# Kernel optimization log

Hardware: AMD Instinct MI355X
Metric: run time of the kernel (lower is better)

Reference implementation:

```python
import jax, jax.numpy as jnp
import numpy as np

MAX_FPS = 30.0
NUM_HEADS = 8


def _rope(x, times):
    # x: [B, H, T, D] with D even; interleaved rotary (even/odd pairs)
    B, H, T, D = x.shape
    inv_freq = 1.0 / (10000.0 ** (jnp.arange(0, D, 2, dtype=jnp.float32) / D))  # [D/2]
    pos = jnp.round(times * MAX_FPS)                       # [B, T]
    freqs = pos[:, :, None] * inv_freq[None, None, :]      # [B, T, D/2]
    cos = jnp.cos(freqs)[:, None, :, :]                    # [B, 1, T, D/2]
    sin = jnp.sin(freqs)[:, None, :, :]
    xp = x.reshape(B, H, T, D // 2, 2)
    x0, x1 = xp[..., 0], xp[..., 1]                        # even-index, odd-index elems
    r0 = x0 * cos - x1 * sin
    r1 = x0 * sin + x1 * cos
    return jnp.stack([r0, r1], axis=-1).reshape(B, H, T, D)


def setup_inputs() -> dict:
    key = jax.random.key(0)
    k1, k2, k3, k4, k5 = jax.random.split(key, 5)
    B, N, C = 4, 2048, 512
    x = jax.random.normal(k1, (B, N, C), dtype=jnp.float32)
    mask = jnp.zeros((B, N), dtype=jnp.float32)  # additive mask, 0 = attend
    # times in seconds; rounded to frame indices inside RoPE
    times = jax.random.uniform(k2, (B, N), dtype=jnp.float32) * (N / MAX_FPS)
    bound_qkv = float(np.sqrt(6.0 / (C + 3 * C)))
    Wqkv = jax.random.uniform(k3, (3 * C, C), minval=-bound_qkv, maxval=bound_qkv, dtype=jnp.float32)
    bound_p = float(np.sqrt(6.0 / (C + C)))
    Wproj = jax.random.uniform(k4, (C, C), minval=-bound_p, maxval=bound_p, dtype=jnp.float32)
    bproj = jnp.zeros((C,), dtype=jnp.float32)
    return {"x": x, "mask": mask, "times": times, "Wqkv": Wqkv,
            "Wproj": Wproj, "bproj": bproj, "num_cls_token": 0}


def reference(x, mask, times, Wqkv, Wproj, bproj, num_cls_token):
    B, N, C = x.shape
    H = NUM_HEADS
    Dh = C // H
    qkv = (x @ Wqkv.T).reshape(B, N, 3, H, Dh).transpose(2, 0, 3, 1, 4)  # [3,B,H,N,Dh]
    q, k, v = qkv[0], qkv[1], qkv[2]
    if num_cls_token > 0:
        c_q, q = q[:, :, :num_cls_token], q[:, :, num_cls_token:]
        c_k, k = k[:, :, :num_cls_token], k[:, :, num_cls_token:]
        t = times
        q = _rope(q, t)
        k = _rope(k, t)
        q = jnp.concatenate([c_q, q], axis=2)
        k = jnp.concatenate([c_k, k], axis=2)
    else:
        q = _rope(q, times)
        k = _rope(k, times)
    scale = 1.0 / jnp.sqrt(jnp.float32(Dh))
    scores = jnp.einsum('bhqd,bhkd->bhqk', q, k) * scale + mask[:, None, None, :]
    attn = jax.nn.softmax(scores, axis=-1)
    out = jnp.einsum('bhqk,bhkd->bhqd', attn, v)           # [B,H,N,Dh]
    out = out.transpose(0, 2, 1, 3).reshape(B, N, C)
    return out @ Wproj.T + bproj
```

## Files before the change

kernel.cpp:

```cpp
#include <hip/hip_runtime.h>
#include <math.h>

#define BB 4
#define NN 2048
#define CC 512
#define HH 8
#define DH 64
#define MM (BB*NN)
#define QKV_N (3*CC)
#define NSP 2
#define SLICE ((size_t)32 * NN)

typedef _Float16 f16;
typedef __attribute__((ext_vector_type(2))) _Float16 f16x2;
typedef __attribute__((ext_vector_type(4))) _Float16 f16x4;
typedef __attribute__((ext_vector_type(8))) _Float16 f16x8;
typedef __attribute__((ext_vector_type(4))) float f32x4;
typedef __attribute__((ext_vector_type(2))) __fp16 h16x2;

#define L2E 1.4426950408889634f
#define QSCL (0.125f * L2E)

__device__ __forceinline__ float fast_exp2(float x) {
#if __has_builtin(__builtin_amdgcn_exp2f)
    return __builtin_amdgcn_exp2f(x);
#else
    float r;
    asm volatile("v_exp_f32 %0, %1\n\ts_nop 1" : "=v"(r) : "v"(x));
    return r;
#endif
}

__device__ __forceinline__ float fdot2(f16x2 a, f16x2 b, float c) {
#if __has_builtin(__builtin_amdgcn_fdot2)
    return __builtin_amdgcn_fdot2(a, b, c, false);
#else
    return c + (float)a[0]*(float)b[0] + (float)a[1]*(float)b[1];
#endif
}

#define GL16(g, l) __builtin_amdgcn_global_load_lds(                       \
    (const __attribute__((address_space(1))) void*)(g),                    \
    (__attribute__((address_space(3))) void*)(l), 16, 0, 0)

#define SX4 (MM*CC/4)
#define SW4 (QKV_N*CC/4)
#define SP4 (CC*CC/4)
#define CAST_T (SX4 + SW4 + SP4)
#define TAB_T (MM * 32)
#define WT_T  (MM / 8)
__global__ __launch_bounds__(256) void cast_tab_kernel(
    const float* __restrict__ x, const float* __restrict__ wqkv,
    const float* __restrict__ wproj, const float* __restrict__ times,
    const float* __restrict__ mask,
    f16* __restrict__ xh, f16* __restrict__ wqh, f16* __restrict__ wph,
    float2* __restrict__ tab, f16* __restrict__ wtab)
{
    const int t = blockIdx.x * 256 + threadIdx.x;
    if (t < CAST_T) {
        const float* src; f16* dst; int i;
        bool qscale = false;
        if (t < SX4)            { src = x;     dst = xh;  i = t; }
        else if (t < SX4 + SW4) { src = wqkv;  dst = wqh; i = t - SX4;
                                  qscale = (i < CC*CC/4); }
        else                    { src = wproj; dst = wph; i = t - SX4 - SW4; }
        f32x4 v = *(const f32x4*)(src + 4 * (size_t)i);
        if (qscale) v *= QSCL;
        f16x4 h = { (f16)v[0], (f16)v[1], (f16)v[2], (f16)v[3] };
        *(f16x4*)(dst + 4 * (size_t)i) = h;
    } else if (t < CAST_T + TAB_T) {
        const int idx = t - CAST_T;
        const int row = idx >> 5, fi = idx & 31;
        const float pos = rintf(times[row] * 30.0f);
        const float invf = exp2f((float)fi * (-13.287712379549449f / 32.0f));
        float s, c;
        sincosf(pos * invf, &s, &c);
        tab[idx] = make_float2(c, s);
    } else {
        const int i = t - CAST_T - TAB_T;
        f32x4 m0 = *(const f32x4*)(mask + 8 * (size_t)i);
        f32x4 m1 = *(const f32x4*)(mask + 8 * (size_t)i + 4);
        f16x8 wv;
        #pragma unroll
        for (int r = 0; r < 4; ++r) {
            wv[r]     = (f16)fast_exp2(m0[r] * L2E);
            wv[4 + r] = (f16)fast_exp2(m1[r] * L2E);
        }
        *(f16x8*)(wtab + 8 * (size_t)i) = wv;
    }
}

__global__ __launch_bounds__(256) void qkv_gemm(
    const f16* __restrict__ xh, const f16* __restrict__ wh,
    const float2* __restrict__ tab, const int* __restrict__ nclsp,
    const f16* __restrict__ wtab,
    f16* __restrict__ qo, f16* __restrict__ ksw, f16* __restrict__ vsw)
{
    __shared__ __align__(16) char smem[32768];
    f16 (*As0)[32] = (f16 (*)[32])smem;
    f16 (*Bs0)[32] = (f16 (*)[32])(smem + 8192);
    f16 (*As1)[32] = (f16 (*)[32])(smem + 16384);
    f16 (*Bs1)[32] = (f16 (*)[32])(smem + 24576);

    const int m0 = blockIdx.x * 128;
    const int n0 = blockIdx.y * 128;
    const int tid = threadIdx.x;
    const int lane = tid & 63;
    const int w = tid >> 6;
    const int wm = (w & 1) * 64, wn = (w >> 1) * 64;
    const int l15 = lane & 15, quad = lane >> 4;

    const int sr = tid >> 2;
    const int sc = (tid & 3) * 8;
    const f16* ga0 = xh + (size_t)(m0 + sr) * CC + sc;
    const f16* ga1 = xh + (size_t)(m0 + sr + 64) * CC + sc;
    const f16* gb0 = wh + (size_t)(n0 + sr) * CC + sc;
    const f16* gb1 = wh + (size_t)(n0 + sr + 64) * CC + sc;

    f32x4 acc[4][4] = {};

    GL16(ga0, &As0[sr][sc]);
    GL16(ga1, &As0[sr + 64][sc]);
    GL16(gb0, &Bs0[sr][sc]);
    GL16(gb1, &Bs0[sr + 64][sc]);

    auto step = [&](int k0, f16 (*Asc)[32], f16 (*Bsc)[32],
                    f16 (*Asn)[32], f16 (*Bsn)[32]) {
        __syncthreads();
        if (k0 + 32 < CC) {
            GL16(ga0 + k0 + 32, &Asn[sr][sc]);
            GL16(ga1 + k0 + 32, &Asn[sr + 64][sc]);
            GL16(gb0 + k0 + 32, &Bsn[sr][sc]);
            GL16(gb1 + k0 + 32, &Bsn[sr + 64][sc]);
        }
        f16x8 af[4], bf[4];
        #pragma unroll
        for (int mi = 0; mi < 4; ++mi)
            af[mi] = *(const f16x8*)&Asc[wm + mi*16 + l15][quad * 8];
        #pragma unroll
        for (int ni = 0; ni < 4; ++ni)
            bf[ni] = *(const f16x8*)&Bsc[wn + ni*16 + l15][quad * 8];
        #pragma unroll
        for (int mi = 0; mi < 4; ++mi)
            #pragma unroll
            for (int ni = 0; ni < 4; ++ni)
                acc[mi][ni] = __builtin_amdgcn_mfma_f32_16x16x32_f16(
                    af[mi], bf[ni], acc[mi][ni], 0, 0, 0);
    };
    #pragma unroll
    for (int kk = 0; kk < CC; kk += 64) {
        step(kk,      As0, Bs0, As1, Bs1);
        step(kk + 32, As1, Bs1, As0, Bs0);
    }
    __syncthreads();

    const int which = n0 >> 9;
    const int b     = m0 >> 11;
    const int mloc  = m0 & (NN - 1);
    const int hbase = (n0 & 511) >> 6;

    if (which < 2) {
        f16 (*Tr)[132] = (f16 (*)[132])smem;
        const int ncls = *nclsp;
        #pragma unroll
        for (int c = 0; c < 2; ++c) {
            if ((w & 1) == c) {
                #pragma unroll
                for (int mi = 0; mi < 4; ++mi)
                    #pragma unroll
                    for (int ni = 0; ni < 4; ++ni)
                        #pragma unroll
                        for (int r = 0; r < 4; ++r)
                            Tr[16*mi + quad*4 + r][wn + 16*ni + l15] =
                                (f16)acc[mi][ni][r];
            }
            __syncthreads();
            const int row = tid >> 2, cg = tid & 3;
            const int n   = mloc + c*64 + row;
            const int hh  = hbase + (cg >> 1);
            const int d0  = (cg & 1) * 32;
            f16x8 vv[4];
            #pragma unroll
            for (int j = 0; j < 4; ++j)
                vv[j] = *(const f16x8*)&Tr[row][cg*32 + j*8];
            if (n >= ncls) {
                const f32x4* t4 = (const f32x4*)(tab + ((size_t)b*NN + n)*32
                                                 + (d0 >> 1));
                #pragma unroll
                for (int j = 0; j < 4; ++j) {
                    f32x4 cs0 = t4[2*j];
                    f32x4 cs1 = t4[2*j + 1];
                    #pragma unroll
                    for (int p = 0; p < 4; ++p) {
                        const float co = (p < 2) ? cs0[(p & 1)*2]
                                                 : cs1[(p & 1)*2];
                        const float s  = (p < 2) ? cs0[(p & 1)*2 + 1]
                                                 : cs1[(p & 1)*2 + 1];
                        const float x0 = (float)vv[j][2*p];
                        const float x1 = (float)vv[j][2*p+1];
                        vv[j][2*p]   = (f16)(x0*co - x1*s);
                        vv[j][2*p+1] = (f16)(x0*s + x1*co);
                    }
                }
            }
            if (which == 0) {
                f16* qp = qo + (((size_t)(b*HH + hh))*NN + n)*DH + d0;
                #pragma unroll
                for (int j = 0; j < 4; ++j)
                    *(f16x8*)(qp + 8*j) = vv[j];
            } else {
                const int ktile = (mloc >> 6) + c;
                f16* kp = ksw + ((((size_t)(b*HH + hh))*32 + ktile)*64 + row)*64;
                #pragma unroll
                for (int j = 0; j < 4; ++j) {
                    const int blk = (d0 >> 3) + j;
                    *(f16x8*)(kp + ((blk ^ (row & 7)) * 8)) = vv[j];
                }
            }
            if (c == 0) __syncthreads();
        }
        return;
    }

    f16 (*Tv)[66] = (f16 (*)[66])smem;
    #pragma unroll
    for (int c = 0; c < 2; ++c) {
        if ((w & 1) == c) {
            #pragma unroll
            for (int mi = 0; mi < 4; ++mi)
                #pragma unroll
                for (int ni = 0; ni < 4; ++ni) {
                    f16x4 pk = { (f16)acc[mi][ni][0], (f16)acc[mi][ni][1],
                                 (f16)acc[mi][ni][2], (f16)acc[mi][ni][3] };
                    *(f16x4*)&Tv[wn + 16*ni + l15][16*mi + quad*4] = pk;
                }
        }
        __syncthreads();
        const int rr = tid >> 1;
        const int d  = rr & 63, hh = hbase + (rr >> 6);
        const int g  = tid & 1;
        const int ktile = (mloc >> 6) + c;
        const size_t wbase = (size_t)b*NN + mloc + c*64;
        f16* vp = vsw + ((((size_t)(b*HH + hh))*32 + ktile)*64 + d)*64;
        #pragma unroll
        for (int j = 0; j < 4; ++j) {
            const int nb  = g*4 + j;
            const int k0l = g*32 + j*4;
            f16x4 lo = *(const f16x4*)&Tv[rr][k0l];
            f16x4 hi = *(const f16x4*)&Tv[rr][k0l + 16];
            lo *= *(const f16x4*)&wtab[wbase + k0l];
            hi *= *(const f16x4*)&wtab[wbase + k0l + 16];
            f16x8 t = __builtin_shufflevector(lo, hi, 0, 1, 2, 3, 4, 5, 6, 7);
            *(f16x8*)(vp + ((nb ^ (d & 7)) * 8)) = t;
        }
        if (c == 0) __syncthreads();
    }
}

__global__ __launch_bounds__(256, 4) void attn_kernel(
    const f16* __restrict__ qg, const f16* __restrict__ ksw,
    const f16* __restrict__ vsw, const f16* __restrict__ wtab,
    f16* __restrict__ On, float* __restrict__ lbuf)
{
    __shared__ __align__(16) f16 asm_[4][4096];

    const int bh = blockIdx.x, qt = blockIdx.y, sp = blockIdx.z;
    const int b = bh >> 3;
    const int tid = threadIdx.x;
    const int w = tid >> 6, lane = tid & 63;
    const int l15 = lane & 15, quad = lane >> 4;
    const int rho = l15 & 7;

    const f16* qbase = qg + ((size_t)bh * NN + qt*128 + w*32) * DH;
    const f16* kt0 = ksw + ((size_t)bh * 32 + sp*16) * 4096;
    const f16* vt0 = vsw + ((size_t)bh * 32 + sp*16) * 4096;
    const f16* wsl = wtab + (size_t)b * NN + sp*1024;

    f16x8 Bq[2][2];
    #pragma unroll
    for (int ni = 0; ni < 2; ++ni)
        #pragma unroll
        for (int kc = 0; kc < 2; ++kc)
            Bq[ni][kc] = *(const f16x8*)(qbase + (size_t)(16*ni + l15) * DH
                                         + kc*32 + quad*8);

    const f32x4 fz = {};
    f32x4 O[2][4] = {};
    float accL[2] = {};

    {
        const f16* ks = kt0 + tid*8;
        const f16* vs = vt0 + tid*8;
        GL16(ks,        &asm_[0][tid*8]);
        GL16(ks + 2048, &asm_[0][2048 + tid*8]);
        GL16(vs,        &asm_[1][tid*8]);
        GL16(vs + 2048, &asm_[1][2048 + tid*8]);
    }

    for (int kt = 0; kt < 16; ++kt) {
        const int cur = (kt & 1) * 2;
        __syncthreads();
        if (kt + 1 < 16) {
            const int nxt = 2 - cur;
            const f16* ks = kt0 + (size_t)(kt+1)*4096 + tid*8;
            const f16* vs = vt0 + (size_t)(kt+1)*4096 + tid*8;
            GL16(ks,        &asm_[nxt][tid*8]);
            GL16(ks + 2048, &asm_[nxt][2048 + tid*8]);
            GL16(vs,        &asm_[nxt+1][tid*8]);
            GL16(vs + 2048, &asm_[nxt+1][2048 + tid*8]);
        }
        const f16 (*Kh)[64] = (const f16 (*)[64])asm_[cur];
        const f16 (*Vt)[64] = (const f16 (*)[64])asm_[cur + 1];

        f32x4 st[4][2];
        const int aw = (quad ^ rho) * 8;
        __builtin_amdgcn_s_setprio(1);
        #pragma unroll
        for (int mi = 0; mi < 4; ++mi) {
            f16x8 Ak0 = *(const f16x8*)&Kh[16*mi + l15][aw];
            f16x8 Ak1 = *(const f16x8*)&Kh[16*mi + l15][aw ^ 32];
            #pragma unroll
            for (int ni = 0; ni < 2; ++ni) {
                f32x4 t0 = __builtin_amdgcn_mfma_f32_16x16x32_f16(
                    Ak0, Bq[ni][0], fz, 0, 0, 0);
                st[mi][ni] = __builtin_amdgcn_mfma_f32_16x16x32_f16(
                    Ak1, Bq[ni][1], t0, 0, 0, 0);
            }
        }
        __builtin_amdgcn_s_setprio(0);

        f16x4 ph[4][2];
        #pragma unroll
        for (int mi = 0; mi < 4; ++mi) {
            #pragma unroll
            for (int ni = 0; ni < 2; ++ni) {
                float e0 = fast_exp2(st[mi][ni][0]);
                float e1 = fast_exp2(st[mi][ni][1]);
                float e2 = fast_exp2(st[mi][ni][2]);
                float e3 = fast_exp2(st[mi][ni][3]);
                h16x2 lo = __builtin_amdgcn_cvt_pkrtz(e0, e1);
                h16x2 hi = __builtin_amdgcn_cvt_pkrtz(e2, e3);
                f16x2 lo2 = __builtin_bit_cast(f16x2, lo);
                f16x2 hi2 = __builtin_bit_cast(f16x2, hi);
                ph[mi][ni] = __builtin_shufflevector(lo2, hi2, 0, 1, 2, 3);
            }
            f16x4 wv = *(const f16x4*)(wsl + kt*64 + 16*mi + quad*4);
            f16x2 wlo = __builtin_shufflevector(wv, wv, 0, 1);
            f16x2 whi = __builtin_shufflevector(wv, wv, 2, 3);
            #pragma unroll
            for (int ni = 0; ni < 2; ++ni) {
                f16x2 plo = __builtin_shufflevector(ph[mi][ni], ph[mi][ni], 0, 1);
                f16x2 phi = __builtin_shufflevector(ph[mi][ni], ph[mi][ni], 2, 3);
                accL[ni] = fdot2(plo, wlo, accL[ni]);
                accL[ni] = fdot2(phi, whi, accL[ni]);
            }
        }

        __builtin_amdgcn_s_setprio(1);
        #pragma unroll
        for (int g = 0; g < 2; ++g) {
            f16x8 p0 = __builtin_shufflevector(ph[2*g][0], ph[2*g+1][0],
                                               0, 1, 2, 3, 4, 5, 6, 7);
            f16x8 p1 = __builtin_shufflevector(ph[2*g][1], ph[2*g+1][1],
                                               0, 1, 2, 3, 4, 5, 6, 7);
            const int vb = ((g*4 + quad) ^ rho) * 8;
            #pragma unroll
            for (int nd = 0; nd < 4; ++nd) {
                f16x8 Av = *(const f16x8*)&Vt[16*nd + l15][vb];
                O[0][nd] = __builtin_amdgcn_mfma_f32_16x16x32_f16(
                    Av, p0, O[0][nd], 0, 0, 0);
                O[1][nd] = __builtin_amdgcn_mfma_f32_16x16x32_f16(
                    Av, p1, O[1][nd], 0, 0, 0);
            }
        }
        __builtin_amdgcn_s_setprio(0);
    }

    #pragma unroll
    for (int ni = 0; ni < 2; ++ni) {
        float l = accL[ni];
        l += __shfl_xor(l, 16);
        l += __shfl_xor(l, 32);
        const float inv = 1.0f / l;
        const int qrow = qt*128 + w*32 + 16*ni + l15;
        const size_t rbase = (size_t)sp * SLICE + (size_t)bh * NN + qrow;
        f16* obase = On + rbase * DH;
        #pragma unroll
        for (int nd = 0; nd < 4; ++nd) {
            f32x4 o = O[ni][nd] * inv;
            f16x4 oh = { (f16)o[0], (f16)o[1], (f16)o[2], (f16)o[3] };
            *(f16x4*)(obase + 16*nd + quad*4) = oh;
        }
        if (quad == 0)
            lbuf[rbase] = l;
    }
}

__global__ __launch_bounds__(256) void proj_gemm(
    const f16* __restrict__ On, const float* __restrict__ lbuf,
    const f16* __restrict__ wh, const float* __restrict__ bias,
    float* __restrict__ out)
{
    __shared__ __align__(16) f16 As[2][128][32];
    __shared__ __align__(16) f16 Bs[2][64][32];
    const int m0 = blockIdx.x * 128;
    const int n0 = blockIdx.y * 64;
    const int tid = threadIdx.x;
    const int lane = tid & 63;
    const int w = tid >> 6;
    const int wm = (w & 1) * 64, wn = (w >> 1) * 32;
    const int l15 = lane & 15, quad = lane >> 4;

    const int b  = m0 >> 11;
    const int q0 = m0 & (NN - 1);

    const int sr = tid >> 2;
    const int sc = (tid & 3) * 8;
    const f16* gb0 = wh + (size_t)(n0 + sr) * CC + sc;

    f16x8 pa0[2], pa1[2];
    float pl0[2], pl1[2];
    auto loadA = [&](int k0) {
        const int h  = k0 >> 6;
        const int d0 = k0 & 63;
        const size_t row0 = (size_t)(b*HH + h) * NN + q0 + sr;
        #pragma unroll
        for (int rr = 0; rr < 2; ++rr) {
            const size_t row = row0 + rr*64;
            pl0[rr] = lbuf[row];
            pl1[rr] = lbuf[SLICE + row];
            pa0[rr] = *(const f16x8*)(On + row * DH + d0 + sc);
            pa1[rr] = *(const f16x8*)(On + (SLICE + row) * DH + d0 + sc);
        }
    };

    f32x4 acc[4][2] = {};

    auto step = [&](int k0, f16 (*Asc)[32], f16 (*Bsc)[32], f16 (*Bsn)[32]) {
        #pragma unroll
        for (int rr = 0; rr < 2; ++rr) {
            const float inv = 1.0f / (pl0[rr] + pl1[rr]);
            const float w0 = pl0[rr] * inv, w1 = pl1[rr] * inv;
            f16x8 o;
            #pragma unroll
            for (int r = 0; r < 8; ++r)
                o[r] = (f16)(w0 * (float)pa0[rr][r] + w1 * (float)pa1[rr][r]);
            *(f16x8*)&Asc[sr + rr*64][sc] = o;
        }
        __syncthreads();
        if (k0 + 32 < CC) {
            GL16(gb0 + k0 + 32, &Bsn[sr][sc]);
            loadA(k0 + 32);
        }
        f16x8 af[4], bf[2];
        #pragma unroll
        for (int mi = 0; mi < 4; ++mi)
            af[mi] = *(const f16x8*)&Asc[wm + mi*16 + l15][quad * 8];
        #pragma unroll
        for (int ni = 0; ni < 2; ++ni)
            bf[ni] = *(const f16x8*)&Bsc[wn + ni*16 + l15][quad * 8];
        #pragma unroll
        for (int mi = 0; mi < 4; ++mi)
            #pragma unroll
            for (int ni = 0; ni < 2; ++ni)
                acc[mi][ni] = __builtin_amdgcn_mfma_f32_16x16x32_f16(
                    af[mi], bf[ni], acc[mi][ni], 0, 0, 0);
    };

    loadA(0);
    GL16(gb0, &Bs[0][sr][sc]);
    #pragma unroll
    for (int kk = 0; kk < CC; kk += 64) {
        step(kk,      As[0], Bs[0], Bs[1]);
        step(kk + 32, As[1], Bs[1], Bs[0]);
    }

    float bb[2];
    #pragma unroll
    for (int ni = 0; ni < 2; ++ni)
        bb[ni] = bias[n0 + wn + ni*16 + l15];

    #pragma unroll
    for (int mi = 0; mi < 4; ++mi)
        #pragma unroll
        for (int r = 0; r < 4; ++r) {
            const int m = m0 + wm + mi*16 + quad*4 + r;
            #pragma unroll
            for (int ni = 0; ni < 2; ++ni)
                out[(size_t)m * CC + n0 + wn + ni*16 + l15] = acc[mi][ni][r] + bb[ni];
        }
}

extern "C" void kernel_launch(void* const* d_in, const int* in_sizes, int n_in,
                              void* d_out, int out_size, void* d_ws, size_t ws_size,
                              hipStream_t stream)
{
    const float* x     = (const float*)d_in[0];
    const float* mask  = (const float*)d_in[1];
    const float* times = (const float*)d_in[2];
    const float* Wqkv  = (const float*)d_in[3];
    const float* Wproj = (const float*)d_in[4];
    const float* bproj = (const float*)d_in[5];
    const int*   ncls  = (const int*)d_in[6];
    float* out = (float*)d_out;

    const size_t per = (size_t)BB * HH * NN * DH;
    f16* xh  = (f16*)d_ws;
    f16* wqh = xh + per;
    f16* wph = wqh + (size_t)QKV_N * CC;
    f16* q   = wph + (size_t)CC * CC;
    f16* ks  = q + per;
    f16* vs  = ks + per;
    f16* On  = vs + per;
    float* lb = (float*)(On + NSP * per);
    float2* tab = (float2*)(lb + NSP * 32 * NN);
    f16* wtab = (f16*)(tab + (size_t)MM * 32);

    cast_tab_kernel<<<(CAST_T + TAB_T + WT_T) / 256, 256, 0, stream>>>(
        x, Wqkv, Wproj, times, mask, xh, wqh, wph, tab, wtab);
    qkv_gemm<<<dim3(MM / 128, QKV_N / 128), 256, 0, stream>>>(
        xh, wqh, tab, ncls, wtab, q, ks, vs);
    attn_kernel<<<dim3(BB * HH, NN / 128, NSP), 256, 0, stream>>>(
        q, ks, vs, wtab, On, lb);
    proj_gemm<<<dim3(MM / 128, CC / 64), 256, 0, stream>>>(
        On, lb, wph, bproj, out);
}
```

Before: 165.3 us.

## Split attention KV into four slices and use 512-thread blocks over 256 queries

Raises the KV split count from 2 to 4 and doubles the attention block to 512 threads (8 waves, 256 query rows). Each K/V tile loaded into shared memory is now shared by twice as many waves, and each thread issues one load per tile instead of two. The projection GEMM is generalised to merge NSP partial outputs, so it now reads four partial slices and normalisers. The aim is better K/V reuse and more parallelism per head. The cost is more partial-output traffic and merge work, and the tighter launch bounds (512, 8) risk register spills.

```diff
diff --git a/kernel.cpp b/kernel.cpp
--- a/kernel.cpp
+++ b/kernel.cpp
@@ -8,7 +8,7 @@
 #define DH 64
 #define MM (BB*NN)
 #define QKV_N (3*CC)
-#define NSP 2
+#define NSP 4
 #define SLICE ((size_t)32 * NN)
 
 typedef _Float16 f16;
@@ -257,7 +257,7 @@
     }
 }
 
-__global__ __launch_bounds__(256, 4) void attn_kernel(
+__global__ __launch_bounds__(512, 8) void attn_kernel(
     const f16* __restrict__ qg, const f16* __restrict__ ksw,
     const f16* __restrict__ vsw, const f16* __restrict__ wtab,
     f16* __restrict__ On, float* __restrict__ lbuf)
@@ -271,10 +271,10 @@
     const int l15 = lane & 15, quad = lane >> 4;
     const int rho = l15 & 7;
 
-    const f16* qbase = qg + ((size_t)bh * NN + qt*128 + w*32) * DH;
-    const f16* kt0 = ksw + ((size_t)bh * 32 + sp*16) * 4096;
-    const f16* vt0 = vsw + ((size_t)bh * 32 + sp*16) * 4096;
-    const f16* wsl = wtab + (size_t)b * NN + sp*1024;
+    const f16* qbase = qg + ((size_t)bh * NN + qt*256 + w*32) * DH;
+    const f16* kt0 = ksw + ((size_t)bh * 32 + sp*8) * 4096;
+    const f16* vt0 = vsw + ((size_t)bh * 32 + sp*8) * 4096;
+    const f16* wsl = wtab + (size_t)b * NN + sp*512;
 
     f16x8 Bq[2][2];
     #pragma unroll
@@ -288,26 +288,16 @@
     f32x4 O[2][4] = {};
     float accL[2] = {};
 
-    {
-        const f16* ks = kt0 + tid*8;
-        const f16* vs = vt0 + tid*8;
-        GL16(ks,        &asm_[0][tid*8]);
-        GL16(ks + 2048, &asm_[0][2048 + tid*8]);
-        GL16(vs,        &asm_[1][tid*8]);
-        GL16(vs + 2048, &asm_[1][2048 + tid*8]);
-    }
-
-    for (int kt = 0; kt < 16; ++kt) {
+    GL16(kt0 + tid*8, &asm_[0][tid*8]);
+    GL16(vt0 + tid*8, &asm_[1][tid*8]);
+
+    for (int kt = 0; kt < 8; ++kt) {
         const int cur = (kt & 1) * 2;
         __syncthreads();
-        if (kt + 1 < 16) {
+        if (kt + 1 < 8) {
             const int nxt = 2 - cur;
-            const f16* ks = kt0 + (size_t)(kt+1)*4096 + tid*8;
-            const f16* vs = vt0 + (size_t)(kt+1)*4096 + tid*8;
-            GL16(ks,        &asm_[nxt][tid*8]);
-            GL16(ks + 2048, &asm_[nxt][2048 + tid*8]);
-            GL16(vs,        &asm_[nxt+1][tid*8]);
-            GL16(vs + 2048, &asm_[nxt+1][2048 + tid*8]);
+            GL16(kt0 + (size_t)(kt+1)*4096 + tid*8, &asm_[nxt][tid*8]);
+            GL16(vt0 + (size_t)(kt+1)*4096 + tid*8, &asm_[nxt+1][tid*8]);
         }
         const f16 (*Kh)[64] = (const f16 (*)[64])asm_[cur];
         const f16 (*Vt)[64] = (const f16 (*)[64])asm_[cur + 1];
@@ -382,7 +372,7 @@
         l += __shfl_xor(l, 16);
         l += __shfl_xor(l, 32);
         const float inv = 1.0f / l;
-        const int qrow = qt*128 + w*32 + 16*ni + l15;
+        const int qrow = qt*256 + w*32 + 16*ni + l15;
         const size_t rbase = (size_t)sp * SLICE + (size_t)bh * NN + qrow;
         f16* obase = On + rbase * DH;
         #pragma unroll
@@ -418,8 +408,8 @@
     const int sc = (tid & 3) * 8;
     const f16* gb0 = wh + (size_t)(n0 + sr) * CC + sc;
 
-    f16x8 pa0[2], pa1[2];
-    float pl0[2], pl1[2];
+    f16x8 pa[NSP][2];
+    float pl[NSP][2];
     auto loadA = [&](int k0) {
         const int h  = k0 >> 6;
         const int d0 = k0 & 63;
@@ -427,10 +417,12 @@
         #pragma unroll
         for (int rr = 0; rr < 2; ++rr) {
             const size_t row = row0 + rr*64;
-            pl0[rr] = lbuf[row];
-            pl1[rr] = lbuf[SLICE + row];
-            pa0[rr] = *(const f16x8*)(On + row * DH + d0 + sc);
-            pa1[rr] = *(const f16x8*)(On + (SLICE + row) * DH + d0 + sc);
+            #pragma unroll
+            for (int s = 0; s < NSP; ++s) {
+                pl[s][rr] = lbuf[(size_t)s * SLICE + row];
+                pa[s][rr] = *(const f16x8*)(On + ((size_t)s * SLICE + row) * DH
+                                            + d0 + sc);
+            }
         }
     };
 
@@ -439,12 +431,22 @@
     auto step = [&](int k0, f16 (*Asc)[32], f16 (*Bsc)[32], f16 (*Bsn)[32]) {
         #pragma unroll
         for (int rr = 0; rr < 2; ++rr) {
-            const float inv = 1.0f / (pl0[rr] + pl1[rr]);
-            const float w0 = pl0[rr] * inv, w1 = pl1[rr] * inv;
+            float lsum = pl[0][rr];
+            #pragma unroll
+            for (int s = 1; s < NSP; ++s) lsum += pl[s][rr];
+            const float inv = 1.0f / lsum;
+            float ws[NSP];
+            #pragma unroll
+            for (int s = 0; s < NSP; ++s) ws[s] = pl[s][rr] * inv;
             f16x8 o;
             #pragma unroll
-            for (int r = 0; r < 8; ++r)
-                o[r] = (f16)(w0 * (float)pa0[rr][r] + w1 * (float)pa1[rr][r]);
+            for (int r = 0; r < 8; ++r) {
+                float acc_ = ws[0] * (float)pa[0][rr][r];
+                #pragma unroll
+                for (int s = 1; s < NSP; ++s)
+                    acc_ += ws[s] * (float)pa[s][rr][r];
+                o[r] = (f16)acc_;
+            }
             *(f16x8*)&Asc[sr + rr*64][sc] = o;
         }
         __syncthreads();
@@ -520,7 +522,7 @@
         x, Wqkv, Wproj, times, mask, xh, wqh, wph, tab, wtab);
     qkv_gemm<<<dim3(MM / 128, QKV_N / 128), 256, 0, stream>>>(
         xh, wqh, tab, ncls, wtab, q, ks, vs);
-    attn_kernel<<<dim3(BB * HH, NN / 128, NSP), 256, 0, stream>>>(
+    attn_kernel<<<dim3(BB * HH, NN / 256, NSP), 512, 0, stream>>>(
         q, ks, vs, wtab, On, lb);
     proj_gemm<<<dim3(MM / 128, CC / 64), 256, 0, stream>>>(
         On, lb, wph, bproj, out);
```

Result: slower. 336.5 us (+103.5%).

## Software-pipeline attention: overlap previous tile's PV MFMA with current exp

Applied to the files above, without the earlier changes.

Restructures the attention inner loop so the P·V matrix multiply for tile kt-1 is issued right after the QK^T MFMAs for tile kt, while the exponentials for tile kt are computed afterwards. V tiles move to a triple-buffered shared array and K stays double-buffered, so the previous V tile is still valid when consumed. This aims to let the matrix units run while the exp/convert work runs on the vector units. It raises LDS use from 32KB to 40KB per block and keeps P live across iterations, which can increase register pressure and may reduce occupancy under the 4-blocks launch bound.

```diff
diff --git a/kernel.cpp b/kernel.cpp
--- a/kernel.cpp
+++ b/kernel.cpp
@@ -262,7 +262,8 @@
     const f16* __restrict__ vsw, const f16* __restrict__ wtab,
     f16* __restrict__ On, float* __restrict__ lbuf)
 {
-    __shared__ __align__(16) f16 asm_[4][4096];
+    __shared__ __align__(16) f16 kbuf[2][4096];
+    __shared__ __align__(16) f16 vbuf[3][4096];
 
     const int bh = blockIdx.x, qt = blockIdx.y, sp = blockIdx.z;
     const int b = bh >> 3;
@@ -287,30 +288,32 @@
     const f32x4 fz = {};
     f32x4 O[2][4] = {};
     float accL[2] = {};
+    f16x4 pP[4][2] = {};
 
     {
         const f16* ks = kt0 + tid*8;
         const f16* vs = vt0 + tid*8;
-        GL16(ks,        &asm_[0][tid*8]);
-        GL16(ks + 2048, &asm_[0][2048 + tid*8]);
-        GL16(vs,        &asm_[1][tid*8]);
-        GL16(vs + 2048, &asm_[1][2048 + tid*8]);
-    }
-
+        GL16(ks,        &kbuf[0][tid*8]);
+        GL16(ks + 2048, &kbuf[0][2048 + tid*8]);
+        GL16(vs,        &vbuf[0][tid*8]);
+        GL16(vs + 2048, &vbuf[0][2048 + tid*8]);
+    }
+
+    int vc = 0;
     for (int kt = 0; kt < 16; ++kt) {
-        const int cur = (kt & 1) * 2;
+        const int kcur = kt & 1;
+        const int vnx = (vc == 2) ? 0 : vc + 1;
+        const int vpv = (vc == 0) ? 2 : vc - 1;
         __syncthreads();
         if (kt + 1 < 16) {
-            const int nxt = 2 - cur;
             const f16* ks = kt0 + (size_t)(kt+1)*4096 + tid*8;
             const f16* vs = vt0 + (size_t)(kt+1)*4096 + tid*8;
-            GL16(ks,        &asm_[nxt][tid*8]);
-            GL16(ks + 2048, &asm_[nxt][2048 + tid*8]);
-            GL16(vs,        &asm_[nxt+1][tid*8]);
-            GL16(vs + 2048, &asm_[nxt+1][2048 + tid*8]);
-        }
-        const f16 (*Kh)[64] = (const f16 (*)[64])asm_[cur];
-        const f16 (*Vt)[64] = (const f16 (*)[64])asm_[cur + 1];
+            GL16(ks,        &kbuf[kcur ^ 1][tid*8]);
+            GL16(ks + 2048, &kbuf[kcur ^ 1][2048 + tid*8]);
+            GL16(vs,        &vbuf[vnx][tid*8]);
+            GL16(vs + 2048, &vbuf[vnx][2048 + tid*8]);
+        }
+        const f16 (*Kh)[64] = (const f16 (*)[64])kbuf[kcur];
 
         f32x4 st[4][2];
         const int aw = (quad ^ rho) * 8;
@@ -327,9 +330,28 @@
                     Ak1, Bq[ni][1], t0, 0, 0, 0);
             }
         }
+
+        if (kt > 0) {
+            const f16 (*Vp)[64] = (const f16 (*)[64])vbuf[vpv];
+            #pragma unroll
+            for (int g = 0; g < 2; ++g) {
+                f16x8 p0 = __builtin_shufflevector(pP[2*g][0], pP[2*g+1][0],
+                                                   0, 1, 2, 3, 4, 5, 6, 7);
+                f16x8 p1 = __builtin_shufflevector(pP[2*g][1], pP[2*g+1][1],
+                                                   0, 1, 2, 3, 4, 5, 6, 7);
+                const int vb = ((g*4 + quad) ^ rho) * 8;
+                #pragma unroll
+                for (int nd = 0; nd < 4; ++nd) {
+                    f16x8 Av = *(const f16x8*)&Vp[16*nd + l15][vb];
+                    O[0][nd] = __builtin_amdgcn_mfma_f32_16x16x32_f16(
+                        Av, p0, O[0][nd], 0, 0, 0);
+                    O[1][nd] = __builtin_amdgcn_mfma_f32_16x16x32_f16(
+                        Av, p1, O[1][nd], 0, 0, 0);
+                }
+            }
+        }
         __builtin_amdgcn_s_setprio(0);
 
-        f16x4 ph[4][2];
         #pragma unroll
         for (int mi = 0; mi < 4; ++mi) {
             #pragma unroll
@@ -342,31 +364,36 @@
                 h16x2 hi = __builtin_amdgcn_cvt_pkrtz(e2, e3);
                 f16x2 lo2 = __builtin_bit_cast(f16x2, lo);
                 f16x2 hi2 = __builtin_bit_cast(f16x2, hi);
-                ph[mi][ni] = __builtin_shufflevector(lo2, hi2, 0, 1, 2, 3);
+                pP[mi][ni] = __builtin_shufflevector(lo2, hi2, 0, 1, 2, 3);
             }
             f16x4 wv = *(const f16x4*)(wsl + kt*64 + 16*mi + quad*4);
             f16x2 wlo = __builtin_shufflevector(wv, wv, 0, 1);
             f16x2 whi = __builtin_shufflevector(wv, wv, 2, 3);
             #pragma unroll
             for (int ni = 0; ni < 2; ++ni) {
-                f16x2 plo = __builtin_shufflevector(ph[mi][ni], ph[mi][ni], 0, 1);
-                f16x2 phi = __builtin_shufflevector(ph[mi][ni], ph[mi][ni], 2, 3);
+                f16x2 plo = __builtin_shufflevector(pP[mi][ni], pP[mi][ni], 0, 1);
+                f16x2 phi = __builtin_shufflevector(pP[mi][ni], pP[mi][ni], 2, 3);
                 accL[ni] = fdot2(plo, wlo, accL[ni]);
                 accL[ni] = fdot2(phi, whi, accL[ni]);
             }
         }
-
+        vc = vnx;
+    }
+
+    {
+        const int vpv = (vc == 0) ? 2 : vc - 1;
+        const f16 (*Vp)[64] = (const f16 (*)[64])vbuf[vpv];
         __builtin_amdgcn_s_setprio(1);
         #pragma unroll
         for (int g = 0; g < 2; ++g) {
-            f16x8 p0 = __builtin_shufflevector(ph[2*g][0], ph[2*g+1][0],
+            f16x8 p0 = __builtin_shufflevector(pP[2*g][0], pP[2*g+1][0],
                                                0, 1, 2, 3, 4, 5, 6, 7);
-            f16x8 p1 = __builtin_shufflevector(ph[2*g][1], ph[2*g+1][1],
+            f16x8 p1 = __builtin_shufflevector(pP[2*g][1], pP[2*g+1][1],
                                                0, 1, 2, 3, 4, 5, 6, 7);
             const int vb = ((g*4 + quad) ^ rho) * 8;
             #pragma unroll
             for (int nd = 0; nd < 4; ++nd) {
-                f16x8 Av = *(const f16x8*)&Vt[16*nd + l15][vb];
+                f16x8 Av = *(const f16x8*)&Vp[16*nd + l15][vb];
                 O[0][nd] = __builtin_amdgcn_mfma_f32_16x16x32_f16(
                     Av, p0, O[0][nd], 0, 0, 0);
                 O[1][nd] = __builtin_amdgcn_mfma_f32_16x16x32_f16(
```

Result: no change. 165.9 us (+0.3%).
